# Kernel optimization log

Hardware: AMD Instinct MI355X
Metric: run time of the kernel (lower is better)

Reference implementation:

```python
import jax, jax.numpy as jnp
import numpy as np

N_NODES = 20000
N_EDGES = 100000
WIDTH = 64
KER_IN = 6
KER_HID = WIDTH // 4  # 16
DEPTH = 6


def setup_inputs() -> dict:
    key = jax.random.key(0)
    ks = jax.random.split(key, 12)
    s = lambda fan_in: 1.0 / np.sqrt(fan_in)
    return {
        "x": jax.random.normal(ks[0], (N_NODES, 1), dtype=jnp.float32),
        "edge_index": jax.random.randint(ks[1], (2, N_EDGES), 0, N_NODES, dtype=jnp.int32),
        "edge_attr": jax.random.uniform(ks[2], (N_EDGES, KER_IN), dtype=jnp.float32),
        "fc1_w": jax.random.normal(ks[3], (1, WIDTH), dtype=jnp.float32) * s(1),
        "fc1_b": jnp.zeros((WIDTH,), dtype=jnp.float32),
        "k1_w": jax.random.normal(ks[4], (KER_IN, KER_HID), dtype=jnp.float32) * s(KER_IN),
        "k1_b": jnp.zeros((KER_HID,), dtype=jnp.float32),
        "k2_w": jax.random.normal(ks[5], (KER_HID, WIDTH * WIDTH), dtype=jnp.float32) * s(KER_HID),
        "k2_b": jnp.zeros((WIDTH * WIDTH,), dtype=jnp.float32),
        "root_w": jax.random.normal(ks[6], (WIDTH, WIDTH), dtype=jnp.float32) * s(WIDTH),
        "conv_b": jnp.zeros((WIDTH,), dtype=jnp.float32),
        "fc2_w": jax.random.normal(ks[7], (WIDTH, 1), dtype=jnp.float32) * s(WIDTH),
        "fc2_b": jnp.zeros((1,), dtype=jnp.float32),
    }


def reference(x, edge_index, edge_attr, fc1_w, fc1_b, k1_w, k1_b, k2_w, k2_b,
              root_w, conv_b, fc2_w, fc2_b):
    src = edge_index[0]  # source nodes j
    dst = edge_index[1]  # target nodes i

    # fc1: lift node features [N,1] -> [N,W]
    h = x @ fc1_w + fc1_b

    # Edge-conditioned weight matrices via kernel MLP (edge_attr is layer-invariant,
    # so compute once and reuse for all DEPTH layers — identical math).
    ek = jax.nn.relu(edge_attr @ k1_w + k1_b)           # [E, W/4]
    W = (ek @ k2_w + k2_b).reshape(N_EDGES, WIDTH, WIDTH)  # [E, W, W]

    # mean aggregation denominator (in-degree, clamped to avoid div-by-zero)
    deg = jax.ops.segment_sum(jnp.ones((N_EDGES,), dtype=h.dtype), dst,
                              num_segments=N_NODES)
    denom = jnp.maximum(deg, 1.0)[:, None]               # [N,1]

    for _ in range(DEPTH):
        # per-edge matmul: msg_e = x_src[e] @ W_e
        msg = jnp.einsum('ei,eio->eo', h[src], W)        # [E, W]
        agg = jax.ops.segment_sum(msg, dst, num_segments=N_NODES) / denom
        h = jax.nn.relu(agg + h @ root_w + conv_b)       # NNConv root weight + bias, then outer ReLU

    return h @ fc2_w + fc2_b                              # [N, 1]
```

## Files before the change

### kernel.cpp

```cpp
#include <hip/hip_runtime.h>
#include <hip/hip_bf16.h>


#define NN 20000
#define NE 100000
#define WD 64
#define DEPTH 6
#define TM 12
#define LSTR 1092

typedef __attribute__((ext_vector_type(8))) short bf16x8;
typedef __attribute__((ext_vector_type(4))) float f32x4;

__device__ __forceinline__ unsigned short f2bf(float v) {
    union { float f; unsigned u; } x; x.f = v;
    unsigned r = x.u + 0x7fffu + ((x.u >> 16) & 1u);
    return (unsigned short)(r >> 16);
}
__device__ __forceinline__ float bf2f(unsigned short b) {
    union { unsigned u; float f; } x; x.u = ((unsigned)b) << 16;
    return x.f;
}

__global__ __launch_bounds__(256) void count_kernel(const int* __restrict__ ei,
                                                    int* __restrict__ outc,
                                                    int* __restrict__ inc)
{
    int e = blockIdx.x * 256 + threadIdx.x;
    if (e >= NE) return;
    atomicAdd(&outc[ei[e]], 1);
    atomicAdd(&inc[ei[NE + e]], 1);
}

__global__ __launch_bounds__(256) void scanA_kernel(const int* __restrict__ cnt,
                                                    int* __restrict__ partials)
{
    int b = blockIdx.x, t = threadIdx.x, lane = t & 63, w = t >> 6;
    int base = b * 1024 + t * 4;
    int s = 0;
#pragma unroll
    for (int i = 0; i < 4; ++i) {
        int idx = base + i;
        if (idx < 2 * NN) s += cnt[idx];
    }
#pragma unroll
    for (int off = 32; off > 0; off >>= 1) s += __shfl_down(s, off, 64);
    __shared__ int wsum[4];
    if (lane == 0) wsum[w] = s;
    __syncthreads();
    if (t == 0) partials[b] = wsum[0] + wsum[1] + wsum[2] + wsum[3];
}

__global__ __launch_bounds__(64) void scanB_kernel(const int* __restrict__ partials,
                                                   int* __restrict__ bases)
{
    int l = threadIdx.x;
    int p = (l < 40) ? partials[l] : 0;
    int v = p;
#pragma unroll
    for (int off = 1; off < 64; off <<= 1) {
        int u = __shfl_up(v, off, 64);
        if (l >= off) v += u;
    }
    if (l < 40) bases[l] = v - p;
}

__global__ __launch_bounds__(256) void scanC_kernel(const int* __restrict__ cnt,
                                                    const int* __restrict__ bases,
                                                    int* __restrict__ rps,
                                                    int* __restrict__ rpd,
                                                    float* __restrict__ invd)
{
    int b = blockIdx.x, t = threadIdx.x, lane = t & 63, w = t >> 6;
    int base = b * 1024 + t * 4;
    int v[4], s = 0;
#pragma unroll
    for (int i = 0; i < 4; ++i) {
        int idx = base + i;
        v[i] = (idx < 2 * NN) ? cnt[idx] : 0;
        s += v[i];
    }
    int tsum = s, sc = s;
#pragma unroll
    for (int off = 1; off < 64; off <<= 1) {
        int u = __shfl_up(sc, off, 64);
        if (lane >= off) sc += u;
    }
    __shared__ int wtot[4];
    if (lane == 63) wtot[w] = sc;
    __syncthreads();
    int wbase = 0;
    for (int j = 0; j < w; ++j) wbase += wtot[j];
    int run = bases[b] + wbase + sc - tsum;
#pragma unroll
    for (int i = 0; i < 4; ++i) {
        int idx = base + i;
        int e = run; run += v[i];
        if (idx < NN) {
            rps[idx] = e;
        } else if (idx < 2 * NN) {
            rpd[idx - NN] = e - NE;
            invd[idx - NN] = 1.0f / fmaxf((float)v[i], 1.0f);
        }
    }
    if (b == 0 && t == 0) { rps[NN] = NE; rpd[NN] = NE; }
}

__global__ __launch_bounds__(256) void ekfill_kernel(
    const int* __restrict__ ei, const float* __restrict__ ea,
    const float* __restrict__ k1w, const float* __restrict__ k1b,
    const int* __restrict__ rps, const int* __restrict__ rpd,
    int* __restrict__ fs, int* __restrict__ fd,
    float* __restrict__ eks, int* __restrict__ ss2sd)
{
    int e = blockIdx.x * 256 + threadIdx.x;
    if (e >= NE) return;
    int s = ei[e], d = ei[NE + e];
    float a[6];
#pragma unroll
    for (int i = 0; i < 6; ++i) a[i] = ea[e * 6 + i];
    int slot_s = rps[s] + atomicAdd(&fs[s], 1);
    int slot_d = rpd[d] + atomicAdd(&fd[d], 1);
    ss2sd[slot_s] = slot_d;
#pragma unroll
    for (int j = 0; j < 16; ++j) {
        float v = k1b[j];
#pragma unroll
        for (int i = 0; i < 6; ++i) v = fmaf(a[i], k1w[i * 16 + j], v);
        eks[(size_t)slot_s * 16 + j] = fmaxf(v, 0.f);
    }
}

__global__ __launch_bounds__(256) void gwt_kernel(
    const float* __restrict__ k2w, const float* __restrict__ k2b,
    const float* __restrict__ rootw,
    unsigned short* __restrict__ Gh, unsigned short* __restrict__ Gl)
{
    int idx = blockIdx.x * 256 + threadIdx.x;
    if (idx >= 1152 * 64) return;
    int n = idx >> 6, k = idx & 63;
    int b = n >> 6, o = n & 63;
    float g;
    if (b < 16)       g = k2w[b * 4096 + k * 64 + o];
    else if (b == 16) g = k2b[k * 64 + o];
    else              g = rootw[k * 64 + o];
    unsigned short hi = f2bf(g);
    Gh[idx] = hi;
    Gl[idx] = f2bf(g - bf2f(hi));
}

__global__ __launch_bounds__(256) void h0_kernel(
    const float* __restrict__ x, const float* __restrict__ w,
    const float* __restrict__ b,
    unsigned short* __restrict__ hhi, unsigned short* __restrict__ hlo)
{
    int idx = blockIdx.x * 256 + threadIdx.x;
    if (idx >= NN * WD) return;
    int n = idx >> 6, o = idx & 63;
    float v = fmaf(x[n], w[o], b[o]);
    unsigned short hi = f2bf(v);
    hhi[idx] = hi;
    hlo[idx] = f2bf(v - bf2f(hi));
}

__global__ __launch_bounds__(256) void gemmsg_kernel(
    const unsigned short* __restrict__ hhi, const unsigned short* __restrict__ hlo,
    const unsigned short* __restrict__ Gh, const unsigned short* __restrict__ Gl,
    const float* __restrict__ eks, const int* __restrict__ ss2sd,
    const int* __restrict__ rps, float* __restrict__ Proot,
    float* __restrict__ msg)
{
    __shared__ float Pt[TM * LSTR];
    int n0 = blockIdx.x * TM;
    int w = threadIdx.x >> 6, l = threadIdx.x & 63;
    int quad = l >> 4, lr = l & 15;
    int arow = n0 + lr;
    if (arow > NN - 1) arow = NN - 1;
    const bf16x8* pah = (const bf16x8*)(hhi + (size_t)arow * 64 + quad * 8);
    const bf16x8* pal = (const bf16x8*)(hlo + (size_t)arow * 64 + quad * 8);
    bf16x8 ah0 = pah[0], ah1 = pah[4];
    bf16x8 al0 = pal[0], al1 = pal[4];

    for (int st = w; st < 18; st += 4) {
        f32x4 acc[4];
#pragma unroll
        for (int t = 0; t < 4; ++t) acc[t] = (f32x4){0.f, 0.f, 0.f, 0.f};
#pragma unroll
        for (int t = 0; t < 4; ++t) {
            int brow = st * 64 + t * 16 + lr;
            const bf16x8* pbh = (const bf16x8*)(Gh + (size_t)brow * 64 + quad * 8);
            const bf16x8* pbl = (const bf16x8*)(Gl + (size_t)brow * 64 + quad * 8);
            bf16x8 bh0 = pbh[0], bh1 = pbh[4];
            bf16x8 bl0 = pbl[0], bl1 = pbl[4];
            f32x4 a = acc[t];
            a = __builtin_amdgcn_mfma_f32_16x16x32_bf16(ah0, bh0, a, 0, 0, 0);
            a = __builtin_amdgcn_mfma_f32_16x16x32_bf16(ah0, bl0, a, 0, 0, 0);
            a = __builtin_amdgcn_mfma_f32_16x16x32_bf16(al0, bh0, a, 0, 0, 0);
            a = __builtin_amdgcn_mfma_f32_16x16x32_bf16(ah1, bh1, a, 0, 0, 0);
            a = __builtin_amdgcn_mfma_f32_16x16x32_bf16(ah1, bl1, a, 0, 0, 0);
            a = __builtin_amdgcn_mfma_f32_16x16x32_bf16(al1, bh1, a, 0, 0, 0);
            acc[t] = a;
        }
        if (st < 17) {
#pragma unroll
            for (int t = 0; t < 4; ++t)
#pragma unroll
                for (int r = 0; r < 4; ++r) {
                    int row = quad * 4 + r;
                    if (row < TM)
                        Pt[row * LSTR + st * 64 + t * 16 + lr] = acc[t][r];
                }
        } else {
#pragma unroll
            for (int t = 0; t < 4; ++t)
#pragma unroll
                for (int r = 0; r < 4; ++r) {
                    int row = quad * 4 + r;
                    int gn = n0 + row;
                    if (row < TM && gn < NN)
                        Proot[(size_t)gn * 64 + t * 16 + lr] = acc[t][r];
                }
        }
    }
    __syncthreads();

#pragma unroll
    for (int j = 0; j < 3; ++j) {
        int ln = w + 4 * j;
        int gn = n0 + ln;
        if (gn >= NN) break;
        int r0 = rps[gn], r1 = rps[gn + 1];
        if (r0 == r1) continue;
        float p[17];
#pragma unroll
        for (int k = 0; k < 17; ++k) p[k] = Pt[ln * LSTR + k * 64 + l];
        for (int s = r0; s < r1; ++s) {
            float ekv = eks[(size_t)s * 16 + (l & 15)];
            int ds = ss2sd[s];
            float m = p[16];
#pragma unroll
            for (int k = 0; k < 16; ++k) m = fmaf(__shfl(ekv, k, 64), p[k], m);
            msg[(size_t)ds * 64 + l] = m;
        }
    }
}

__global__ __launch_bounds__(256) void agg_kernel(
    const float* __restrict__ msg, const int* __restrict__ rpd,
    const float* __restrict__ invd, const float* __restrict__ Proot,
    const float* __restrict__ convb, float* __restrict__ h,
    unsigned short* __restrict__ hhi, unsigned short* __restrict__ hlo)
{
    int i = blockIdx.x * 4 + (threadIdx.x >> 6);
    if (i >= NN) return;
    int l = threadIdx.x & 63;
    int r0 = rpd[i], r1 = rpd[i + 1];
    float acc = 0.f;
    for (int s = r0; s < r1; ++s) acc += msg[(size_t)s * 64 + l];
    float v = fmaf(acc, invd[i], Proot[(size_t)i * 64 + l] + convb[l]);
    v = fmaxf(v, 0.f);
    int idx = i * 64 + l;
    h[idx] = v;
    unsigned short hi = f2bf(v);
    hhi[idx] = hi;
    hlo[idx] = f2bf(v - bf2f(hi));
}

__global__ __launch_bounds__(256) void out_kernel(
    const float* __restrict__ h, const float* __restrict__ fc2_w,
    const float* __restrict__ fc2_b, float* __restrict__ out)
{
    int wave = blockIdx.x * 4 + (threadIdx.x >> 6);
    int lane = threadIdx.x & 63;
    float v = h[(size_t)wave * 64 + lane] * fc2_w[lane];
#pragma unroll
    for (int off = 32; off > 0; off >>= 1) v += __shfl_down(v, off);
    if (lane == 0) out[wave] = v + fc2_b[0];
}

extern "C" void kernel_launch(void* const* d_in, const int* in_sizes, int n_in,
                              void* d_out, int out_size, void* d_ws, size_t ws_size,
                              hipStream_t stream)
{
    const float* x         = (const float*)d_in[0];
    const int*   ei        = (const int*)  d_in[1];
    const float* edge_attr = (const float*)d_in[2];
    const float* fc1_w     = (const float*)d_in[3];
    const float* fc1_b     = (const float*)d_in[4];
    const float* k1_w      = (const float*)d_in[5];
    const float* k1_b      = (const float*)d_in[6];
    const float* k2_w      = (const float*)d_in[7];
    const float* k2_b      = (const float*)d_in[8];
    const float* root_w    = (const float*)d_in[9];
    const float* conv_b    = (const float*)d_in[10];
    const float* fc2_w     = (const float*)d_in[11];
    const float* fc2_b     = (const float*)d_in[12];
    float* out = (float*)d_out;

    float* ws = (float*)d_ws;
    size_t off = 0;
    int* cnt   = (int*)(ws + off); off += 4 * NN;
    int* outc  = cnt;
    int* inc   = cnt + NN;
    int* fs    = cnt + 2 * NN;
    int* fd    = cnt + 3 * NN;
    int* rps   = (int*)(ws + off); off += 20004;
    int* rpd   = (int*)(ws + off); off += 20004;
    int* partials = (int*)(ws + off); off += 64;
    int* bases    = (int*)(ws + off); off += 64;
    int* ss2sd = (int*)(ws + off); off += NE;
    float* invd  = ws + off; off += NN;
    float* eks   = ws + off; off += (size_t)NE * 16;
    unsigned short* Gh  = (unsigned short*)(ws + off); off += 36864;
    unsigned short* Gl  = (unsigned short*)(ws + off); off += 36864;
    unsigned short* hhi = (unsigned short*)(ws + off); off += (size_t)NN * 32;
    unsigned short* hlo = (unsigned short*)(ws + off); off += (size_t)NN * 32;
    float* h     = ws + off; off += (size_t)NN * WD;
    float* msg   = ws + off; off += (size_t)NE * WD;
    float* Proot = ws + off; off += (size_t)NN * WD;

    hipMemsetAsync(cnt, 0, 4 * NN * sizeof(int), stream);
    count_kernel<<<(NE + 255) / 256, 256, 0, stream>>>(ei, outc, inc);
    scanA_kernel<<<40, 256, 0, stream>>>(cnt, partials);
    scanB_kernel<<<1, 64, 0, stream>>>(partials, bases);
    scanC_kernel<<<40, 256, 0, stream>>>(cnt, bases, rps, rpd, invd);
    ekfill_kernel<<<(NE + 255) / 256, 256, 0, stream>>>(ei, edge_attr, k1_w, k1_b,
                                                        rps, rpd, fs, fd, eks, ss2sd);
    gwt_kernel<<<(1152 * 64 + 255) / 256, 256, 0, stream>>>(k2_w, k2_b, root_w, Gh, Gl);
    h0_kernel<<<(NN * WD + 255) / 256, 256, 0, stream>>>(x, fc1_w, fc1_b, hhi, hlo);

    int ntiles = (NN + TM - 1) / TM;
    for (int layer = 0; layer < DEPTH; ++layer) {
        gemmsg_kernel<<<ntiles, 256, 0, stream>>>(hhi, hlo, Gh, Gl, eks, ss2sd,
                                                  rps, Proot, msg);
        agg_kernel<<<(NN + 3) / 4, 256, 0, stream>>>(msg, rpd, invd, Proot,
                                                     conv_b, h, hhi, hlo);
    }

    out_kernel<<<NN / 4, 256, 0, stream>>>(h, fc2_w, fc2_b, out);
}
```

Before: 694.3 us.

## Balance per-edge message work across waves using slot-to-source map and 512 threads

The per-source message phase now distributes the tile's out-edges evenly over 8 waves through a new slot-to-source index, where before each wave handled whole source nodes. This removes load imbalance caused by varying out-degree. The block grows to 512 threads and the tile to 15 rows, giving more LDS per block and possibly lower occupancy. P values are read from LDS per edge rather than cached in registers, which adds LDS traffic.

```diff
diff --git a/kernel.cpp b/kernel.cpp
--- a/kernel.cpp
+++ b/kernel.cpp
@@ -6,7 +6,7 @@
 #define NE 100000
 #define WD 64
 #define DEPTH 6
-#define TM 12
+#define TM 15
 #define LSTR 1092
 
 typedef __attribute__((ext_vector_type(8))) short bf16x8;
@@ -111,7 +111,8 @@
     const float* __restrict__ k1w, const float* __restrict__ k1b,
     const int* __restrict__ rps, const int* __restrict__ rpd,
     int* __restrict__ fs, int* __restrict__ fd,
-    float* __restrict__ eks, int* __restrict__ ss2sd)
+    float* __restrict__ eks, int* __restrict__ ss2sd,
+    int* __restrict__ slot2src)
 {
     int e = blockIdx.x * 256 + threadIdx.x;
     if (e >= NE) return;
@@ -122,6 +123,7 @@
     int slot_s = rps[s] + atomicAdd(&fs[s], 1);
     int slot_d = rpd[d] + atomicAdd(&fd[d], 1);
     ss2sd[slot_s] = slot_d;
+    slot2src[slot_s] = s;
 #pragma unroll
     for (int j = 0; j < 16; ++j) {
         float v = k1b[j];
@@ -163,14 +165,14 @@
     hlo[idx] = f2bf(v - bf2f(hi));
 }
 
-__global__ __launch_bounds__(256) void gemmsg_kernel(
+__global__ __launch_bounds__(512) void fused_kernel(
     const unsigned short* __restrict__ hhi, const unsigned short* __restrict__ hlo,
     const unsigned short* __restrict__ Gh, const unsigned short* __restrict__ Gl,
     const float* __restrict__ eks, const int* __restrict__ ss2sd,
-    const int* __restrict__ rps, float* __restrict__ Proot,
-    float* __restrict__ msg)
-{
-    __shared__ float Pt[TM * LSTR];
+    const int* __restrict__ slot2src, const int* __restrict__ rps,
+    float* __restrict__ Proot, float* __restrict__ msg)
+{
+    __shared__ __align__(16) float Pt[TM * LSTR];
     int n0 = blockIdx.x * TM;
     int w = threadIdx.x >> 6, l = threadIdx.x & 63;
     int quad = l >> 4, lr = l & 15;
@@ -181,7 +183,7 @@
     bf16x8 ah0 = pah[0], ah1 = pah[4];
     bf16x8 al0 = pal[0], al1 = pal[4];
 
-    for (int st = w; st < 18; st += 4) {
+    for (int st = w; st < 18; st += 8) {
         f32x4 acc[4];
 #pragma unroll
         for (int t = 0; t < 4; ++t) acc[t] = (f32x4){0.f, 0.f, 0.f, 0.f};
@@ -224,24 +226,18 @@
     }
     __syncthreads();
 
-#pragma unroll
-    for (int j = 0; j < 3; ++j) {
-        int ln = w + 4 * j;
-        int gn = n0 + ln;
-        if (gn >= NN) break;
-        int r0 = rps[gn], r1 = rps[gn + 1];
-        if (r0 == r1) continue;
-        float p[17];
-#pragma unroll
-        for (int k = 0; k < 17; ++k) p[k] = Pt[ln * LSTR + k * 64 + l];
-        for (int s = r0; s < r1; ++s) {
-            float ekv = eks[(size_t)s * 16 + (l & 15)];
-            int ds = ss2sd[s];
-            float m = p[16];
-#pragma unroll
-            for (int k = 0; k < 16; ++k) m = fmaf(__shfl(ekv, k, 64), p[k], m);
-            msg[(size_t)ds * 64 + l] = m;
-        }
+    int nend = n0 + TM; if (nend > NN) nend = NN;
+    int r0 = rps[n0], r1 = rps[nend];
+    for (int s = r0 + w; s < r1; s += 8) {
+        int ln = slot2src[s] - n0;
+        float ekv = eks[(size_t)s * 16 + (l & 15)];
+        int ds = ss2sd[s];
+        const float* Pr = &Pt[ln * LSTR];
+        float m = Pr[16 * 64 + l];
+#pragma unroll
+        for (int k = 0; k < 16; ++k)
+            m = fmaf(__shfl(ekv, k, 64), Pr[k * 64 + l], m);
+        msg[(size_t)ds * 64 + l] = m;
     }
 }
 
@@ -308,7 +304,8 @@
     int* rpd   = (int*)(ws + off); off += 20004;
     int* partials = (int*)(ws + off); off += 64;
     int* bases    = (int*)(ws + off); off += 64;
-    int* ss2sd = (int*)(ws + off); off += NE;
+    int* ss2sd    = (int*)(ws + off); off += NE;
+    int* slot2src = (int*)(ws + off); off += NE;
     float* invd  = ws + off; off += NN;
     float* eks   = ws + off; off += (size_t)NE * 16;
     unsigned short* Gh  = (unsigned short*)(ws + off); off += 36864;
@@ -325,14 +322,15 @@
     scanB_kernel<<<1, 64, 0, stream>>>(partials, bases);
     scanC_kernel<<<40, 256, 0, stream>>>(cnt, bases, rps, rpd, invd);
     ekfill_kernel<<<(NE + 255) / 256, 256, 0, stream>>>(ei, edge_attr, k1_w, k1_b,
-                                                        rps, rpd, fs, fd, eks, ss2sd);
+                                                        rps, rpd, fs, fd, eks,
+                                                        ss2sd, slot2src);
     gwt_kernel<<<(1152 * 64 + 255) / 256, 256, 0, stream>>>(k2_w, k2_b, root_w, Gh, Gl);
     h0_kernel<<<(NN * WD + 255) / 256, 256, 0, stream>>>(x, fc1_w, fc1_b, hhi, hlo);
 
     int ntiles = (NN + TM - 1) / TM;
     for (int layer = 0; layer < DEPTH; ++layer) {
-        gemmsg_kernel<<<ntiles, 256, 0, stream>>>(hhi, hlo, Gh, Gl, eks, ss2sd,
-                                                  rps, Proot, msg);
+        fused_kernel<<<ntiles, 512, 0, stream>>>(hhi, hlo, Gh, Gl, eks, ss2sd,
+                                                 slot2src, rps, Proot, msg);
         agg_kernel<<<(NN + 3) / 4, 256, 0, stream>>>(msg, rpd, invd, Proot,
                                                      conv_b, h, hhi, hlo);
     }
```

Measured after the change: 628.2 us. 9.5% less time.
